# Performance work log

Measured on AMD Instinct MI355X. Metric: run time of the kernel, lower is better.

## Reference

```python
import jax, jax.numpy as jnp
import numpy as np

SHIFT = 8
CUR_FRAME = 16
NUM_K = 32
TEMP = 1.0


def wrap_angle(x):
    return (x + jnp.pi) % (2.0 * jnp.pi) - jnp.pi


def setup_inputs() -> dict:
    key = jax.random.key(0)
    k1, k2, k3, k4, k5 = jax.random.split(key, 5)
    A, S, T = 8192, 96, 1024
    valid = jax.random.randint(k1, (A, S), 0, 2).astype(bool)
    pos = jax.random.normal(k2, (A, S, 2), dtype=jnp.float32) * 50.0
    heading = jax.random.uniform(k3, (A, S), minval=-jnp.pi, maxval=jnp.pi, dtype=jnp.float32)
    tok_xy = jax.random.normal(k4, (T, 2), dtype=jnp.float32) * 2.0
    tok_h = jax.random.uniform(k5, (T, 1), minval=-jnp.pi, maxval=jnp.pi, dtype=jnp.float32)
    token_endpoint = jnp.concatenate([tok_xy, tok_h], axis=-1)
    return {"valid": valid, "pos": pos, "heading": heading, "token_endpoint": token_endpoint}


def _clean_heading(valid, heading):
    # sequential fix of >1.5 rad heading jumps (state carried along time)
    valid_pairs = valid[:, :-1] & valid[:, 1:]

    def step(h_prev, x):
        h_next, vp = x
        diff = jnp.abs(wrap_angle(h_prev - h_next))
        change = (diff > 1.5) & vp
        h_new = jnp.where(change, h_prev, h_next)
        return h_new, h_new

    h0 = heading[:, 0]
    _, hs = jax.lax.scan(step, h0, (heading[:, 1:].T, valid_pairs.T))
    return jnp.concatenate([h0[:, None], hs.T], axis=1)


def _extrapolate_stationary(valid, pos, heading):
    A, S = valid.shape
    t = jnp.argmax(valid, axis=1)  # first valid step per agent
    n_fill = t % SHIFT
    special = (t == CUR_FRAME) & (~valid[:, CUR_FRAME - SHIFT])
    n_fill = jnp.where(special, SHIFT, n_fill)
    steps = jnp.arange(S)[None, :]
    mask = (steps >= (t - n_fill)[:, None]) & (steps < t[:, None])  # [A,S]
    ra = jnp.arange(A)
    pos_t = pos[ra, t]          # [A,2]
    head_t = heading[ra, t]     # [A]
    valid = valid | mask
    pos = jnp.where(mask[..., None], pos_t[:, None, :], pos)
    heading = jnp.where(mask, head_t[:, None], heading)
    return valid, pos, heading


def _match_agent_token_center(valid, pos, heading, token_endpoint, key):
    A, S = valid.shape
    tx, ty, th = token_endpoint[:, 0], token_endpoint[:, 1], token_endpoint[:, 2]
    idxs = jnp.arange(SHIFT, S, SHIFT)
    ra = jnp.arange(A)

    def local_to_global(prev_pos, prev_head):
        c, s = jnp.cos(prev_head), jnp.sin(prev_head)
        gx = c[:, None] * tx[None, :] - s[:, None] * ty[None, :] + prev_pos[:, 0:1]
        gy = s[:, None] * tx[None, :] + c[:, None] * ty[None, :] + prev_pos[:, 1:2]
        return gx, gy  # each [A, n_token]

    def step(carry, x):
        prev_pos, prev_head, prev_pos_s, prev_head_s, key = carry
        v_prev, v_cur, pos_i, head_i = x
        key, sk = jax.random.split(key)
        _valid = v_prev & v_cur

        # --- greedy (gt) branch ---
        gx, gy = local_to_global(prev_pos, prev_head)
        dist = (gx - pos_i[:, 0:1]) ** 2 + (gy - pos_i[:, 1:2]) ** 2
        idx_gt = jnp.argmin(dist, axis=-1)
        new_pos_gt = jnp.stack([gx[ra, idx_gt], gy[ra, idx_gt]], axis=-1)
        new_head_gt = wrap_angle(prev_head + th[idx_gt])
        prev_pos = jnp.where(_valid[:, None], new_pos_gt, pos_i)
        prev_head = jnp.where(_valid, new_head_gt, head_i)
        gt_pos_o = jnp.where(_valid[:, None], prev_pos, 0.0)
        gt_head_o = jnp.where(_valid, prev_head, 0.0)

        # --- sampled branch (num_k > 1) ---
        gxs, gys = local_to_global(prev_pos_s, prev_head_s)
        dist_s = (gxs - pos_i[:, 0:1]) ** 2 + (gys - pos_i[:, 1:2]) ** 2
        neg_top, top_idx = jax.lax.top_k(-dist_s, NUM_K)  # smallest distances
        logits = neg_top / TEMP  # == -dist / temp
        samp = jax.random.categorical(sk, logits, axis=-1)
        idx_s = jnp.take_along_axis(top_idx, samp[:, None], axis=1)[:, 0]
        new_pos_s = jnp.stack([gxs[ra, idx_s], gys[ra, idx_s]], axis=-1)
        new_head_s = wrap_angle(prev_head_s + th[idx_s])
        prev_pos_s = jnp.where(_valid[:, None], new_pos_s, pos_i)
        prev_head_s = jnp.where(_valid, new_head_s, head_i)
        s_pos_o = jnp.where(_valid[:, None], prev_pos_s, 0.0)
        s_head_o = jnp.where(_valid, prev_head_s, 0.0)

        new_carry = (prev_pos, prev_head, prev_pos_s, prev_head_s, key)
        return new_carry, (_valid, idx_gt, gt_pos_o, gt_head_o, idx_s, s_pos_o, s_head_o)

    init = (pos[:, 0], heading[:, 0], pos[:, 0], heading[:, 0], key)
    xs = (valid[:, idxs - SHIFT].T,
          valid[:, idxs].T,
          jnp.moveaxis(pos[:, idxs], 1, 0),
          heading[:, idxs].T)
    _, ys = jax.lax.scan(step, init, xs)
    # move step axis from 0 to 1 -> [A, n_out_steps, ...]
    return tuple(jnp.moveaxis(y, 0, 1) for y in ys)


def reference(valid, pos, heading, token_endpoint):
    heading = _clean_heading(valid, heading)
    valid, pos, heading = _extrapolate_stationary(valid, pos, heading)
    return _match_agent_token_center(valid, pos, heading, token_endpoint, jax.random.key(42))
```

## Files before the change

### kernel.cpp

```cpp
#include <hip/hip_runtime.h>
#include <math.h>

#define NTOK 1024
#define NSTEPS 11

typedef __attribute__((ext_vector_type(2))) float f32x2;

__device__ __forceinline__ float fadd_(float a, float b){ return __fadd_rn(a,b); }
__device__ __forceinline__ float fsub_(float a, float b){ return __fsub_rn(a,b); }
__device__ __forceinline__ float fmul_(float a, float b){ return __fmul_rn(a,b); }

__device__ __forceinline__ float wrap_angle(float x){
  const float PI_F     = 3.14159265358979323846f;
  const float TWO_PI_F = 6.28318530717958647692f;
  float t = fadd_(x, PI_F);
  float r = (t >= TWO_PI_F) ? fsub_(t, TWO_PI_F) : t;
  if (r < 0.0f) r = fadd_(r, TWO_PI_F);
  return fsub_(r, PI_F);
}

__device__ __forceinline__ void tf2x32(unsigned k0, unsigned k1,
                                       unsigned c0, unsigned c1,
                                       unsigned &o0, unsigned &o1){
  unsigned ks2 = k0 ^ k1 ^ 0x1BD11BDAu;
  unsigned x0 = c0 + k0, x1 = c1 + k1;
#define TFR(r) { x0 += x1; x1 = (x1 << (r)) | (x1 >> (32 - (r))); x1 ^= x0; }
  TFR(13) TFR(15) TFR(26) TFR(6)   x0 += k1;  x1 += ks2 + 1u;
  TFR(17) TFR(29) TFR(16) TFR(24)  x0 += ks2; x1 += k0  + 2u;
  TFR(13) TFR(15) TFR(26) TFR(6)   x0 += k0;  x1 += k1  + 3u;
  TFR(17) TFR(29) TFR(16) TFR(24)  x0 += k1;  x1 += ks2 + 4u;
  TFR(13) TFR(15) TFR(26) TFR(6)   x0 += ks2; x1 += k0  + 5u;
#undef TFR
  o0 = x0; o1 = x1;
}

static void tf2x32_host(unsigned k0, unsigned k1, unsigned c0, unsigned c1,
                        unsigned &o0, unsigned &o1){
  unsigned ks2 = k0 ^ k1 ^ 0x1BD11BDAu;
  unsigned x0 = c0 + k0, x1 = c1 + k1;
#define TFR(r) { x0 += x1; x1 = (x1 << (r)) | (x1 >> (32 - (r))); x1 ^= x0; }
  TFR(13) TFR(15) TFR(26) TFR(6)   x0 += k1;  x1 += ks2 + 1u;
  TFR(17) TFR(29) TFR(16) TFR(24)  x0 += ks2; x1 += k0  + 2u;
  TFR(13) TFR(15) TFR(26) TFR(6)   x0 += k0;  x1 += k1  + 3u;
  TFR(17) TFR(29) TFR(16) TFR(24)  x0 += k1;  x1 += ks2 + 4u;
  TFR(13) TFR(15) TFR(26) TFR(6)   x0 += ks2; x1 += k0  + 5u;
#undef TFR
  o0 = x0; o1 = x1;
}

struct StepKeys { unsigned a[2 * NSTEPS]; };

__device__ __forceinline__ float gumbel_from_bits(unsigned bits){
  unsigned m = bits >> 9;
  float u = (m == 0u) ? 1.17549435e-38f
                      : fsub_(__uint_as_float(0x3F800000u | m), 1.0f);
  float l1 = (float)log((double)u);
  float l2 = (float)log((double)(-l1));
  return -l2;
}

__device__ __forceinline__ unsigned wbcast_umin(unsigned x){
  asm("s_nop 1\n\t"
      "v_min_u32_dpp %0, %0, %0 row_shr:1  row_mask:0xf bank_mask:0xf\n\t"
      "s_nop 1\n\t"
      "v_min_u32_dpp %0, %0, %0 row_shr:2  row_mask:0xf bank_mask:0xf\n\t"
      "s_nop 1\n\t"
      "v_min_u32_dpp %0, %0, %0 row_shr:4  row_mask:0xf bank_mask:0xf\n\t"
      "s_nop 1\n\t"
      "v_min_u32_dpp %0, %0, %0 row_shr:8  row_mask:0xf bank_mask:0xf\n\t"
      "s_nop 1\n\t"
      "v_min_u32_dpp %0, %0, %0 row_bcast:15 row_mask:0xa bank_mask:0xf\n\t"
      "s_nop 1\n\t"
      "v_min_u32_dpp %0, %0, %0 row_bcast:31 row_mask:0xc bank_mask:0xf\n\t"
      "s_nop 1"
      : "+v"(x));
  return (unsigned)__builtin_amdgcn_readlane((int)x, 63);
}
__device__ __forceinline__ unsigned wbcast_umax(unsigned x){
  asm("s_nop 1\n\t"
      "v_max_u32_dpp %0, %0, %0 row_shr:1  row_mask:0xf bank_mask:0xf\n\t"
      "s_nop 1\n\t"
      "v_max_u32_dpp %0, %0, %0 row_shr:2  row_mask:0xf bank_mask:0xf\n\t"
      "s_nop 1\n\t"
      "v_max_u32_dpp %0, %0, %0 row_shr:4  row_mask:0xf bank_mask:0xf\n\t"
      "s_nop 1\n\t"
      "v_max_u32_dpp %0, %0, %0 row_shr:8  row_mask:0xf bank_mask:0xf\n\t"
      "s_nop 1\n\t"
      "v_max_u32_dpp %0, %0, %0 row_bcast:15 row_mask:0xa bank_mask:0xf\n\t"
      "s_nop 1\n\t"
      "v_max_u32_dpp %0, %0, %0 row_bcast:31 row_mask:0xc bank_mask:0xf\n\t"
      "s_nop 1"
      : "+v"(x));
  return (unsigned)__builtin_amdgcn_readlane((int)x, 63);
}

#define CE(i,j) { unsigned long long a_ = dp[i], b_ = dp[j]; bool lt_ = a_ < b_; \
                  dp[i] = lt_ ? a_ : b_; dp[j] = lt_ ? b_ : a_; }

extern "C" __global__ void __launch_bounds__(256)
sctoken_kernel(const int* __restrict__ valid,
               const float* __restrict__ pos,
               const float* __restrict__ heading,
               const float* __restrict__ tok,
               float* __restrict__ out,
               StepKeys ks)
{
  __shared__ float2 s_txy[NTOK];
  __shared__ float  s_th[NTOK];
  __shared__ float  s_cpx[4][12], s_cpy[4][12], s_ch[4][12];
  __shared__ int    s_cv[4][12];
  __shared__ unsigned long long s_q[256][15];
  __shared__ unsigned long long s_aux[4][96];

  const int tid = threadIdx.x;
  for (int j = tid; j < NTOK; j += 256) {
    s_txy[j] = make_float2(tok[3*j], tok[3*j+1]);
    s_th[j]  = tok[3*j+2];
  }
  s_q[tid][14] = ~0ULL;
  const int wave = tid >> 6;
  const int lane = tid & 63;
  const int a = blockIdx.x * 4 + wave;

  const int*   va = valid   + a * 96;
  const float* ha = heading + a * 96;
  const float* pa = pos     + a * 192;

  {
    float hprev = ha[0];
    int   vprev = va[0];
    int   t = 0; bool seen = (vprev != 0);
    float ptx = pa[0], pty = pa[1], hth = hprev;
    if (lane == 0) {
      s_cv[wave][0] = vprev; s_cpx[wave][0] = pa[0]; s_cpy[wave][0] = pa[1]; s_ch[wave][0] = hprev;
    }
    for (int s = 1; s < 96; ++s) {
      int vcur = va[s];
      float hn = ha[s];
      float diff = fabsf(wrap_angle(fsub_(hprev, hn)));
      float hnew = ((diff > 1.5f) && vprev && vcur) ? hprev : hn;
      if (!seen && vcur) { seen = true; t = s; ptx = pa[2*s]; pty = pa[2*s+1]; hth = hnew; }
      if (((s & 7) == 0) && (s <= 88) && (lane == 0)) {
        int i = s >> 3;
        s_cv[wave][i] = vcur; s_cpx[wave][i] = pa[2*s]; s_cpy[wave][i] = pa[2*s+1]; s_ch[wave][i] = hnew;
      }
      hprev = hnew; vprev = vcur;
    }
    int n_fill = t & 7;
    if ((t == 16) && (va[8] == 0)) n_fill = 8;
    if ((lane == 0) && (n_fill > 0)) {
      int c = t - n_fill;
      int i = c >> 3;
      s_cv[wave][i] = 1; s_cpx[wave][i] = ptx; s_cpy[wave][i] = pty; s_ch[wave][i] = hth;
    }
  }
  __syncthreads();

  float gpx = s_cpx[wave][0], gpy = s_cpy[wave][0], ghd = s_ch[wave][0];
  float spx = gpx, spy = gpy, shd = ghd;

  #pragma unroll 1
  for (int st = 0; st < NSTEPS; ++st) {
    const unsigned sk0 = ks.a[2*st], sk1 = ks.a[2*st+1];

    const int  vprev  = s_cv[wave][st];
    const int  vcur   = s_cv[wave][st+1];
    const bool valid_ = (vprev != 0) && (vcur != 0);
    const float pix = s_cpx[wave][st+1];
    const float piy = s_cpy[wave][st+1];
    const float hin = s_ch[wave][st+1];
    const int oi = a * NSTEPS + st;

    float g = 0.0f;
    if (lane < 32) {
      unsigned b1, b2;
      tf2x32(sk0, sk1, 0u, (unsigned)(a * 32 + lane), b1, b2);
      g = gumbel_from_bits(b1 ^ b2);
    }

    double sgd, cgd, ssd, csd;
    sincos((double)ghd, &sgd, &cgd);
    sincos((double)shd, &ssd, &csd);
    const float cg = (float)cgd, sg = (float)sgd;
    const float cs2 = (float)csd, ss2 = (float)ssd;

    unsigned dm = 0xffffffffu; unsigned im = 0u;
    unsigned long long dp[16];

    {
      #pragma clang fp contract(off)
      const f32x2 Ag = {cg, sg},  Bg = {-sg, cg};
      const f32x2 As = {cs2, ss2}, Bs = {-ss2, cs2};
      const f32x2 Pg = {gpx, gpy}, Ps = {spx, spy};
      const f32x2 Qn = {-pix, -piy};
      #pragma unroll
      for (int i2 = 0; i2 < 16; ++i2) {
        int j = lane + (i2 << 6);
        float2 t2 = s_txy[j];
        const f32x2 tx = {t2.x, t2.x}, ty = {t2.y, t2.y};
        f32x2 gg = ((Ag * tx) + (Bg * ty)) + Pg;
        f32x2 dg = gg + Qn;
        f32x2 qg = dg * dg;
        float dG = __fadd_rn(qg.x, qg.y);
        unsigned du = __float_as_uint(dG);
        bool lt = du < dm;
        dm = lt ? du : dm;
        im = lt ? (unsigned)j : im;
        f32x2 gs = ((As * tx) + (Bs * ty)) + Ps;
        f32x2 dsv = gs + Qn;
        f32x2 qs = dsv * dsv;
        float dS = __fadd_rn(qs.x, qs.y);
        dp[i2] = (((unsigned long long)__float_as_uint(dS)) << 10) | (unsigned)j;
      }
    }

    {
      unsigned gdm = wbcast_umin(dm);
      unsigned long long m = __ballot(dm == gdm);
      int jgt;
      if (__popcll(m) > 1) {
        unsigned ci = (dm == gdm) ? im : 0xffffffffu;
        jgt = (int)wbcast_umin(ci);
      } else {
        jgt = __builtin_amdgcn_readlane((int)im, __ffsll(m) - 1);
      }
      float2 t2 = s_txy[jgt];
      float gx = fadd_(fsub_(fmul_(cg, t2.x), fmul_(sg, t2.y)), gpx);
      float gy = fadd_(fadd_(fmul_(sg, t2.x), fmul_(cg, t2.y)), gpy);
      float nh = wrap_angle(fadd_(ghd, s_th[jgt]));
      float upx = valid_ ? gx : pix;
      float upy = valid_ ? gy : piy;
      float uhd = valid_ ? nh : hin;
      gpx = upx; gpy = upy; ghd = uhd;
      if (lane == 0) {
        out[oi]                = valid_ ? 1.0f : 0.0f;
        out[90112  + oi]       = (float)jgt;
        out[180224 + 2*oi]     = valid_ ? upx : 0.0f;
        out[180224 + 2*oi + 1] = valid_ ? upy : 0.0f;
        out[360448 + oi]       = valid_ ? uhd : 0.0f;
      }
    }

    {
      CE(0,1) CE(2,3) CE(4,5) CE(6,7) CE(8,9) CE(10,11) CE(12,13) CE(14,15)
      CE(0,2) CE(1,3) CE(4,6) CE(5,7) CE(8,10) CE(9,11) CE(12,14) CE(13,15)
      CE(1,2) CE(5,6) CE(9,10) CE(13,14)
      CE(0,4) CE(1,5) CE(2,6) CE(3,7) CE(8,12) CE(9,13) CE(10,14) CE(11,15)
      CE(2,4) CE(3,5) CE(10,12) CE(11,13)
      CE(1,2) CE(3,4) CE(5,6) CE(9,10) CE(11,12) CE(13,14)
      CE(0,8) CE(1,9) CE(2,10) CE(3,11) CE(4,12) CE(5,13) CE(6,14) CE(7,15)
      CE(4,8) CE(5,9) CE(6,10) CE(7,11)
      CE(2,4) CE(3,5) CE(6,8) CE(7,9) CE(10,12) CE(11,13)
      CE(1,2) CE(3,4) CE(5,6) CE(7,8) CE(9,10) CE(11,12) CE(13,14)

      #pragma unroll
      for (int i2 = 2; i2 < 16; ++i2) s_q[tid][i2-2] = dp[i2];
      unsigned hdist  = (unsigned)(dp[0] >> 10), hidx  = (unsigned)dp[0] & 1023u;
      unsigned h2dist = (unsigned)(dp[1] >> 10), h2idx = (unsigned)dp[1] & 1023u;
      int pops = 0;
      unsigned long long fetchv = s_q[tid][0];

      #pragma unroll 1
      for (int k = 0; k < 32; ++k) {
        unsigned gd = wbcast_umin(hdist);
        unsigned long long m = __ballot(hdist == gd);
        bool own;
        if (__popcll(m) > 1) {
          unsigned ci = (hdist == gd) ? hidx : 0xffffffffu;
          unsigned gi = wbcast_umin(ci);
          own = (hdist == gd) && (hidx == gi);
        } else {
          own = (hdist == gd);
        }
        s_aux[wave][own ? (unsigned)k : 32u + (unsigned)lane] =
            (((unsigned long long)hdist) << 32) | hidx;
        unsigned fd = (unsigned)(fetchv >> 10), fi = (unsigned)fetchv & 1023u;
        hdist  = own ? h2dist : hdist;
        hidx   = own ? h2idx  : hidx;
        h2dist = own ? fd : h2dist;
        h2idx  = own ? fi : h2idx;
        pops   = own ? pops + 1 : pops;
        int slot = pops < 14 ? pops : 14;
        fetchv = s_q[tid][slot];
      }

      unsigned mu = 0u;
      if (lane < 32) {
        unsigned long long v = s_aux[wave][lane];
        float myv = -__uint_as_float((unsigned)(v >> 32));
        float cand = fadd_(myv, g);
        unsigned cu = __float_as_uint(cand);
        mu = (cu & 0x80000000u) ? ~cu : (cu | 0x80000000u);
      }
      unsigned gmu = wbcast_umax(mu);
      unsigned long long m2 = __ballot(mu == gmu);
      int kl = __ffsll(m2) - 1;
      int js = (int)(unsigned)(s_aux[wave][kl] & 0xffffffffULL);
      float2 t2 = s_txy[js];
      float gx = fadd_(fsub_(fmul_(cs2, t2.x), fmul_(ss2, t2.y)), spx);
      float gy = fadd_(fadd_(fmul_(ss2, t2.x), fmul_(cs2, t2.y)), spy);
      float nh = wrap_angle(fadd_(shd, s_th[js]));
      float upx = valid_ ? gx : pix;
      float upy = valid_ ? gy : piy;
      float uhd = valid_ ? nh : hin;
      spx = upx; spy = upy; shd = uhd;
      if (lane == 0) {
        out[450560 + oi]       = (float)js;
        out[540672 + 2*oi]     = valid_ ? upx : 0.0f;
        out[540672 + 2*oi + 1] = valid_ ? upy : 0.0f;
        out[720896 + oi]       = valid_ ? uhd : 0.0f;
      }
    }
  }
}

extern "C" void kernel_launch(void* const* d_in, const int* in_sizes, int n_in,
                              void* d_out, int out_size, void* d_ws, size_t ws_size,
                              hipStream_t stream) {
  const int*   valid   = (const int*)  d_in[0];
  const float* pos     = (const float*)d_in[1];
  const float* heading = (const float*)d_in[2];
  const float* tok     = (const float*)d_in[3];
  float* out           = (float*)d_out;
  (void)in_sizes; (void)n_in; (void)out_size; (void)d_ws; (void)ws_size;

  StepKeys ks;
  unsigned k0 = 0u, k1 = 42u;
  for (int st = 0; st < NSTEPS; ++st) {
    unsigned nk0, nk1, s0, s1;
    tf2x32_host(k0, k1, 0u, 0u, nk0, nk1);
    tf2x32_host(k0, k1, 0u, 1u, s0, s1);
    ks.a[2*st] = s0; ks.a[2*st+1] = s1;
    k0 = nk0; k1 = nk1;
  }

  hipLaunchKernelGGL(sctoken_kernel, dim3(2048), dim3(256), 0, stream,
                     valid, pos, heading, tok, out, ks);
}
```

Measured before the change: 366.4 us.

## Process two agents per wavefront using half-wave reductions and 32-element sorts

Each 64-lane wavefront now handles two agents, one per 32-lane half. Reductions stop at row_bcast:15 and read lanes 31 and 63 separately. Each lane now holds 32 candidates, sorted with a bitonic network, and keeps a four-deep head cache for the top-32 extraction, which halves the number of wavefronts doing the serial 32-iteration selection loop. Token data is read straight from global memory instead of being staged in LDS. The costs are a larger per-lane sort, more registers, and uncached global gathers.

```diff
diff --git a/kernel.cpp b/kernel.cpp
--- a/kernel.cpp
+++ b/kernel.cpp
@@ -59,7 +59,7 @@
   return -l2;
 }
 
-__device__ __forceinline__ unsigned wbcast_umin(unsigned x){
+__device__ __forceinline__ unsigned hmin(unsigned x, int lane){
   asm("s_nop 1\n\t"
       "v_min_u32_dpp %0, %0, %0 row_shr:1  row_mask:0xf bank_mask:0xf\n\t"
       "s_nop 1\n\t"
@@ -70,13 +70,13 @@
       "v_min_u32_dpp %0, %0, %0 row_shr:8  row_mask:0xf bank_mask:0xf\n\t"
       "s_nop 1\n\t"
       "v_min_u32_dpp %0, %0, %0 row_bcast:15 row_mask:0xa bank_mask:0xf\n\t"
-      "s_nop 1\n\t"
-      "v_min_u32_dpp %0, %0, %0 row_bcast:31 row_mask:0xc bank_mask:0xf\n\t"
       "s_nop 1"
       : "+v"(x));
-  return (unsigned)__builtin_amdgcn_readlane((int)x, 63);
-}
-__device__ __forceinline__ unsigned wbcast_umax(unsigned x){
+  unsigned ra = (unsigned)__builtin_amdgcn_readlane((int)x, 31);
+  unsigned rb = (unsigned)__builtin_amdgcn_readlane((int)x, 63);
+  return lane < 32 ? ra : rb;
+}
+__device__ __forceinline__ unsigned hmax(unsigned x, int lane){
   asm("s_nop 1\n\t"
       "v_max_u32_dpp %0, %0, %0 row_shr:1  row_mask:0xf bank_mask:0xf\n\t"
       "s_nop 1\n\t"
@@ -87,17 +87,17 @@
       "v_max_u32_dpp %0, %0, %0 row_shr:8  row_mask:0xf bank_mask:0xf\n\t"
       "s_nop 1\n\t"
       "v_max_u32_dpp %0, %0, %0 row_bcast:15 row_mask:0xa bank_mask:0xf\n\t"
-      "s_nop 1\n\t"
-      "v_max_u32_dpp %0, %0, %0 row_bcast:31 row_mask:0xc bank_mask:0xf\n\t"
       "s_nop 1"
       : "+v"(x));
-  return (unsigned)__builtin_amdgcn_readlane((int)x, 63);
-}
-
-#define CE(i,j) { unsigned long long a_ = dp[i], b_ = dp[j]; bool lt_ = a_ < b_; \
-                  dp[i] = lt_ ? a_ : b_; dp[j] = lt_ ? b_ : a_; }
-
-extern "C" __global__ void __launch_bounds__(256)
+  unsigned ra = (unsigned)__builtin_amdgcn_readlane((int)x, 31);
+  unsigned rb = (unsigned)__builtin_amdgcn_readlane((int)x, 63);
+  return lane < 32 ? ra : rb;
+}
+
+#define CE2(i,j) { unsigned long long a_ = dp[i], b_ = dp[j]; bool lt_ = a_ < b_; \
+                   dp[i] = lt_ ? a_ : b_; dp[j] = lt_ ? b_ : a_; }
+
+extern "C" __global__ void __launch_bounds__(64)
 sctoken_kernel(const int* __restrict__ valid,
                const float* __restrict__ pos,
                const float* __restrict__ heading,
@@ -105,22 +105,17 @@
                float* __restrict__ out,
                StepKeys ks)
 {
-  __shared__ float2 s_txy[NTOK];
-  __shared__ float  s_th[NTOK];
-  __shared__ float  s_cpx[4][12], s_cpy[4][12], s_ch[4][12];
-  __shared__ int    s_cv[4][12];
-  __shared__ unsigned long long s_q[256][15];
-  __shared__ unsigned long long s_aux[4][96];
-
-  const int tid = threadIdx.x;
-  for (int j = tid; j < NTOK; j += 256) {
-    s_txy[j] = make_float2(tok[3*j], tok[3*j+1]);
-    s_th[j]  = tok[3*j+2];
-  }
-  s_q[tid][14] = ~0ULL;
-  const int wave = tid >> 6;
-  const int lane = tid & 63;
-  const int a = blockIdx.x * 4 + wave;
+  __shared__ unsigned long long s_q[64][29];
+  __shared__ unsigned long long s_aux[128];
+  __shared__ float s_cpx[2][12], s_cpy[2][12], s_ch[2][12];
+  __shared__ int   s_cv[2][12];
+
+  const int lane = threadIdx.x;
+  const int half = lane >> 5;
+  const int lh   = lane & 31;
+  const int a    = blockIdx.x * 2 + half;
+
+  s_q[lane][28] = ~0ULL;
 
   const int*   va = valid   + a * 96;
   const float* ha = heading + a * 96;
@@ -131,8 +126,8 @@
     int   vprev = va[0];
     int   t = 0; bool seen = (vprev != 0);
     float ptx = pa[0], pty = pa[1], hth = hprev;
-    if (lane == 0) {
-      s_cv[wave][0] = vprev; s_cpx[wave][0] = pa[0]; s_cpy[wave][0] = pa[1]; s_ch[wave][0] = hprev;
+    if (lh == 0) {
+      s_cv[half][0] = vprev; s_cpx[half][0] = pa[0]; s_cpy[half][0] = pa[1]; s_ch[half][0] = hprev;
     }
     for (int s = 1; s < 96; ++s) {
       int vcur = va[s];
@@ -140,43 +135,41 @@
       float diff = fabsf(wrap_angle(fsub_(hprev, hn)));
       float hnew = ((diff > 1.5f) && vprev && vcur) ? hprev : hn;
       if (!seen && vcur) { seen = true; t = s; ptx = pa[2*s]; pty = pa[2*s+1]; hth = hnew; }
-      if (((s & 7) == 0) && (s <= 88) && (lane == 0)) {
+      if (((s & 7) == 0) && (s <= 88) && (lh == 0)) {
         int i = s >> 3;
-        s_cv[wave][i] = vcur; s_cpx[wave][i] = pa[2*s]; s_cpy[wave][i] = pa[2*s+1]; s_ch[wave][i] = hnew;
+        s_cv[half][i] = vcur; s_cpx[half][i] = pa[2*s]; s_cpy[half][i] = pa[2*s+1]; s_ch[half][i] = hnew;
       }
       hprev = hnew; vprev = vcur;
     }
     int n_fill = t & 7;
     if ((t == 16) && (va[8] == 0)) n_fill = 8;
-    if ((lane == 0) && (n_fill > 0)) {
+    if ((lh == 0) && (n_fill > 0)) {
       int c = t - n_fill;
       int i = c >> 3;
-      s_cv[wave][i] = 1; s_cpx[wave][i] = ptx; s_cpy[wave][i] = pty; s_ch[wave][i] = hth;
+      s_cv[half][i] = 1; s_cpx[half][i] = ptx; s_cpy[half][i] = pty; s_ch[half][i] = hth;
     }
   }
   __syncthreads();
 
-  float gpx = s_cpx[wave][0], gpy = s_cpy[wave][0], ghd = s_ch[wave][0];
+  float gpx = s_cpx[half][0], gpy = s_cpy[half][0], ghd = s_ch[half][0];
   float spx = gpx, spy = gpy, shd = ghd;
 
   #pragma unroll 1
   for (int st = 0; st < NSTEPS; ++st) {
     const unsigned sk0 = ks.a[2*st], sk1 = ks.a[2*st+1];
 
-    const int  vprev  = s_cv[wave][st];
-    const int  vcur   = s_cv[wave][st+1];
+    const int  vprev  = s_cv[half][st];
+    const int  vcur   = s_cv[half][st+1];
     const bool valid_ = (vprev != 0) && (vcur != 0);
-    const float pix = s_cpx[wave][st+1];
-    const float piy = s_cpy[wave][st+1];
-    const float hin = s_ch[wave][st+1];
+    const float pix = s_cpx[half][st+1];
+    const float piy = s_cpy[half][st+1];
+    const float hin = s_ch[half][st+1];
     const int oi = a * NSTEPS + st;
 
-    float g = 0.0f;
-    if (lane < 32) {
-      unsigned b1, b2;
-      tf2x32(sk0, sk1, 0u, (unsigned)(a * 32 + lane), b1, b2);
-      g = gumbel_from_bits(b1 ^ b2);
-    }
+    float g;
+    { unsigned b1, b2;
+      tf2x32(sk0, sk1, 0u, (unsigned)(a * 32 + lh), b1, b2);
+      g = gumbel_from_bits(b1 ^ b2); }
 
     double sgd, cgd, ssd, csd;
     sincos((double)ghd, &sgd, &cgd);
@@ -185,7 +178,7 @@
     const float cs2 = (float)csd, ss2 = (float)ssd;
 
     unsigned dm = 0xffffffffu; unsigned im = 0u;
-    unsigned long long dp[16];
+    unsigned long long dp[32];
 
     {
       #pragma clang fp contract(off)
@@ -194,10 +187,10 @@
       const f32x2 Pg = {gpx, gpy}, Ps = {spx, spy};
       const f32x2 Qn = {-pix, -piy};
       #pragma unroll
-      for (int i2 = 0; i2 < 16; ++i2) {
-        int j = lane + (i2 << 6);
-        float2 t2 = s_txy[j];
-        const f32x2 tx = {t2.x, t2.x}, ty = {t2.y, t2.y};
+      for (int i2 = 0; i2 < 32; ++i2) {
+        int j = lh + (i2 << 5);
+        float tx0 = tok[3*j], ty0 = tok[3*j+1];
+        const f32x2 tx = {tx0, tx0}, ty = {ty0, ty0};
         f32x2 gg = ((Ag * tx) + (Bg * ty)) + Pg;
         f32x2 dg = gg + Qn;
         f32x2 qg = dg * dg;
@@ -215,24 +208,27 @@
     }
 
     {
-      unsigned gdm = wbcast_umin(dm);
+      unsigned gdm = hmin(dm, lane);
       unsigned long long m = __ballot(dm == gdm);
+      unsigned mA = (unsigned)m, mB = (unsigned)(m >> 32);
       int jgt;
-      if (__popcll(m) > 1) {
+      if (__popc(mA) > 1 || __popc(mB) > 1) {
         unsigned ci = (dm == gdm) ? im : 0xffffffffu;
-        jgt = (int)wbcast_umin(ci);
+        jgt = (int)hmin(ci, lane);
       } else {
-        jgt = __builtin_amdgcn_readlane((int)im, __ffsll(m) - 1);
-      }
-      float2 t2 = s_txy[jgt];
-      float gx = fadd_(fsub_(fmul_(cg, t2.x), fmul_(sg, t2.y)), gpx);
-      float gy = fadd_(fadd_(fmul_(sg, t2.x), fmul_(cg, t2.y)), gpy);
-      float nh = wrap_angle(fadd_(ghd, s_th[jgt]));
+        int jA = __builtin_amdgcn_readlane((int)im, __ffs(mA) - 1);
+        int jB = __builtin_amdgcn_readlane((int)im, 32 + (__ffs(mB) - 1));
+        jgt = lane < 32 ? jA : jB;
+      }
+      float tjx = tok[3*jgt], tjy = tok[3*jgt+1], tjh = tok[3*jgt+2];
+      float gx = fadd_(fsub_(fmul_(cg, tjx), fmul_(sg, tjy)), gpx);
+      float gy = fadd_(fadd_(fmul_(sg, tjx), fmul_(cg, tjy)), gpy);
+      float nh = wrap_angle(fadd_(ghd, tjh));
       float upx = valid_ ? gx : pix;
       float upy = valid_ ? gy : piy;
       float uhd = valid_ ? nh : hin;
       gpx = upx; gpy = upy; ghd = uhd;
-      if (lane == 0) {
+      if (lh == 0) {
         out[oi]                = valid_ ? 1.0f : 0.0f;
         out[90112  + oi]       = (float)jgt;
         out[180224 + 2*oi]     = valid_ ? upx : 0.0f;
@@ -242,69 +238,74 @@
     }
 
     {
-      CE(0,1) CE(2,3) CE(4,5) CE(6,7) CE(8,9) CE(10,11) CE(12,13) CE(14,15)
-      CE(0,2) CE(1,3) CE(4,6) CE(5,7) CE(8,10) CE(9,11) CE(12,14) CE(13,15)
-      CE(1,2) CE(5,6) CE(9,10) CE(13,14)
-      CE(0,4) CE(1,5) CE(2,6) CE(3,7) CE(8,12) CE(9,13) CE(10,14) CE(11,15)
-      CE(2,4) CE(3,5) CE(10,12) CE(11,13)
-      CE(1,2) CE(3,4) CE(5,6) CE(9,10) CE(11,12) CE(13,14)
-      CE(0,8) CE(1,9) CE(2,10) CE(3,11) CE(4,12) CE(5,13) CE(6,14) CE(7,15)
-      CE(4,8) CE(5,9) CE(6,10) CE(7,11)
-      CE(2,4) CE(3,5) CE(6,8) CE(7,9) CE(10,12) CE(11,13)
-      CE(1,2) CE(3,4) CE(5,6) CE(7,8) CE(9,10) CE(11,12) CE(13,14)
-
       #pragma unroll
-      for (int i2 = 2; i2 < 16; ++i2) s_q[tid][i2-2] = dp[i2];
-      unsigned hdist  = (unsigned)(dp[0] >> 10), hidx  = (unsigned)dp[0] & 1023u;
-      unsigned h2dist = (unsigned)(dp[1] >> 10), h2idx = (unsigned)dp[1] & 1023u;
+      for (int bp = 1; bp < 32; bp <<= 1) {
+        #pragma unroll
+        for (int bk = bp; bk >= 1; bk >>= 1) {
+          #pragma unroll
+          for (int jj = (bk & (bp - 1)); jj + bk < 32; jj += 2 * bk) {
+            #pragma unroll
+            for (int ii = 0; ii < bk; ++ii) {
+              int lo = jj + ii, hi = jj + ii + bk;
+              if (hi < 32 && (lo / (2 * bp)) == (hi / (2 * bp))) { CE2(lo, hi) }
+            }
+          }
+        }
+      }
+
+      #pragma unroll
+      for (int i2 = 4; i2 < 32; ++i2) s_q[lane][i2-4] = dp[i2];
+      unsigned h1d = (unsigned)(dp[0] >> 10), h1i = (unsigned)dp[0] & 1023u;
+      unsigned h2d = (unsigned)(dp[1] >> 10), h2i = (unsigned)dp[1] & 1023u;
+      unsigned h3d = (unsigned)(dp[2] >> 10), h3i = (unsigned)dp[2] & 1023u;
+      unsigned h4d = (unsigned)(dp[3] >> 10), h4i = (unsigned)dp[3] & 1023u;
       int pops = 0;
-      unsigned long long fetchv = s_q[tid][0];
+      unsigned long long fetchv = s_q[lane][0];
 
       #pragma unroll 1
-      for (int k = 0; k < 32; ++k) {
-        unsigned gd = wbcast_umin(hdist);
-        unsigned long long m = __ballot(hdist == gd);
+      for (int k2 = 0; k2 < 32; ++k2) {
+        unsigned gd = hmin(h1d, lane);
+        unsigned long long m = __ballot(h1d == gd);
+        unsigned mA = (unsigned)m, mB = (unsigned)(m >> 32);
         bool own;
-        if (__popcll(m) > 1) {
-          unsigned ci = (hdist == gd) ? hidx : 0xffffffffu;
-          unsigned gi = wbcast_umin(ci);
-          own = (hdist == gd) && (hidx == gi);
+        if (__popc(mA) > 1 || __popc(mB) > 1) {
+          unsigned ci = (h1d == gd) ? h1i : 0xffffffffu;
+          unsigned gi = hmin(ci, lane);
+          own = (h1d == gd) && (h1i == gi);
         } else {
-          own = (hdist == gd);
+          own = (h1d == gd);
         }
-        s_aux[wave][own ? (unsigned)k : 32u + (unsigned)lane] =
-            (((unsigned long long)hdist) << 32) | hidx;
+        s_aux[own ? (unsigned)((lane & 32) + k2) : (unsigned)(64 + lane)] =
+            (((unsigned long long)h1d) << 32) | h1i;
         unsigned fd = (unsigned)(fetchv >> 10), fi = (unsigned)fetchv & 1023u;
-        hdist  = own ? h2dist : hdist;
-        hidx   = own ? h2idx  : hidx;
-        h2dist = own ? fd : h2dist;
-        h2idx  = own ? fi : h2idx;
-        pops   = own ? pops + 1 : pops;
-        int slot = pops < 14 ? pops : 14;
-        fetchv = s_q[tid][slot];
-      }
-
-      unsigned mu = 0u;
-      if (lane < 32) {
-        unsigned long long v = s_aux[wave][lane];
-        float myv = -__uint_as_float((unsigned)(v >> 32));
-        float cand = fadd_(myv, g);
-        unsigned cu = __float_as_uint(cand);
-        mu = (cu & 0x80000000u) ? ~cu : (cu | 0x80000000u);
-      }
-      unsigned gmu = wbcast_umax(mu);
+        h1d = own ? h2d : h1d;  h1i = own ? h2i : h1i;
+        h2d = own ? h3d : h2d;  h2i = own ? h3i : h2i;
+        h3d = own ? h4d : h3d;  h3i = own ? h4i : h3i;
+        h4d = own ? fd  : h4d;  h4i = own ? fi  : h4i;
+        pops = own ? pops + 1 : pops;
+        int slot = pops < 28 ? pops : 28;
+        fetchv = s_q[lane][slot];
+      }
+
+      unsigned long long v = s_aux[lane];
+      float myv = -__uint_as_float((unsigned)(v >> 32));
+      float cand = fadd_(myv, g);
+      unsigned cu = __float_as_uint(cand);
+      unsigned mu = (cu & 0x80000000u) ? ~cu : (cu | 0x80000000u);
+      unsigned gmu = hmax(mu, lane);
       unsigned long long m2 = __ballot(mu == gmu);
-      int kl = __ffsll(m2) - 1;
-      int js = (int)(unsigned)(s_aux[wave][kl] & 0xffffffffULL);
-      float2 t2 = s_txy[js];
-      float gx = fadd_(fsub_(fmul_(cs2, t2.x), fmul_(ss2, t2.y)), spx);
-      float gy = fadd_(fadd_(fmul_(ss2, t2.x), fmul_(cs2, t2.y)), spy);
-      float nh = wrap_angle(fadd_(shd, s_th[js]));
+      unsigned mA2 = (unsigned)m2, mB2 = (unsigned)(m2 >> 32);
+      int kl = lane < 32 ? (__ffs(mA2) - 1) : 32 + (__ffs(mB2) - 1);
+      int js = (int)(unsigned)(s_aux[kl] & 0xffffffffULL);
+      float tjx = tok[3*js], tjy = tok[3*js+1], tjh = tok[3*js+2];
+      float gx = fadd_(fsub_(fmul_(cs2, tjx), fmul_(ss2, tjy)), spx);
+      float gy = fadd_(fadd_(fmul_(ss2, tjx), fmul_(cs2, tjy)), spy);
+      float nh = wrap_angle(fadd_(shd, tjh));
       float upx = valid_ ? gx : pix;
       float upy = valid_ ? gy : piy;
       float uhd = valid_ ? nh : hin;
       spx = upx; spy = upy; shd = uhd;
-      if (lane == 0) {
+      if (lh == 0) {
         out[450560 + oi]       = (float)js;
         out[540672 + 2*oi]     = valid_ ? upx : 0.0f;
         out[540672 + 2*oi + 1] = valid_ ? upy : 0.0f;
@@ -334,6 +335,6 @@
     k0 = nk0; k1 = nk1;
   }
 
-  hipLaunchKernelGGL(sctoken_kernel, dim3(2048), dim3(256), 0, stream,
+  hipLaunchKernelGGL(sctoken_kernel, dim3(4096), dim3(64), 0, stream,
                      valid, pos, heading, tok, out, ks);
 }
```

Measured after the change: 570.8 us. 55.8% more time.
